# Kernel optimization log

Hardware: AMD Instinct MI355X
Metric: run time of the kernel (lower is better)

The kernel has to match this reference:

```python
import jax, jax.numpy as jnp
import numpy as np

N = 50000      # nodes
E = 1600000    # edges (before self loops)
IN = 128
OUT = 128
H = 4
HD = OUT // H  # head dim = 32


def setup_inputs() -> dict:
    key = jax.random.key(0)
    k1, k2, k3, k4, k5 = jax.random.split(key, 5)
    x = jax.random.normal(k1, (N, IN), dtype=jnp.float32)
    edge_index = jax.random.randint(k2, (2, E), 0, N, dtype=jnp.int64)
    # xavier-uniform-ish scales
    W = jax.random.normal(k3, (OUT, IN), dtype=jnp.float32) * (1.0 / np.sqrt(IN))
    att_src = jax.random.normal(k4, (1, H, HD), dtype=jnp.float32) * 0.1
    att_dst = jax.random.normal(k5, (1, H, HD), dtype=jnp.float32) * 0.1
    return {"x": x, "edge_index": edge_index, "W": W, "att_src": att_src, "att_dst": att_dst}


def reference(x, edge_index, W, att_src, att_dst):
    n = x.shape[0]
    # add self loops (tg.utils.add_self_loops appends [i, i] edges)
    loops = jnp.arange(n, dtype=edge_index.dtype)
    ei = jnp.concatenate([edge_index, jnp.stack([loops, loops])], axis=1)
    src, dst = ei[0], ei[1]

    # linear projection, split into heads: [n, H, HD]
    h = (x @ W.T).reshape(n, H, HD)

    # per-node attention logits per head: [n, H]
    a_src = jnp.sum(h * att_src, axis=-1)
    a_dst = jnp.sum(h * att_dst, axis=-1)

    # per-edge attention score: gather + leaky_relu
    alpha = a_src[src] + a_dst[dst]                      # [Etot, H]
    alpha = jax.nn.leaky_relu(alpha, negative_slope=0.2)

    # segment softmax grouped by destination node (numerically stable)
    m = jax.ops.segment_max(alpha, dst, num_segments=n)  # [n, H]
    e = jnp.exp(alpha - m[dst])
    s = jax.ops.segment_sum(e, dst, num_segments=n)      # [n, H]
    e = e / s[dst]                                       # [Etot, H]

    # weighted scatter-add aggregation; f_additive adds 1 to the weights
    msg = h[src] * (e[:, :, None] + 1.0)                 # [Etot, H, HD]
    out = jax.ops.segment_sum(msg, dst, num_segments=n)  # [n, H, HD]
    return out.reshape(n, -1)
```

## Files before the change

### kernel.cpp

```cpp
#include <hip/hip_runtime.h>

#define N_NODES 50000
#define E_EDGES 1600000
#define ETOT    (E_EDGES + N_NODES)
#define DIN  128
#define DOUT 128
#define NH   4
#define HD   32

typedef unsigned short ushort_t;
typedef unsigned int uint_t;
typedef __attribute__((ext_vector_type(8))) short bfrag;
typedef __attribute__((ext_vector_type(4))) float ffrag;

__device__ __forceinline__ ushort_t f2bf(float f) {
  uint_t u = __float_as_uint(f);
  u += 0x7fffu + ((u >> 16) & 1u);
  return (ushort_t)(u >> 16);
}
__device__ __forceinline__ float bf_lo(uint_t u) {
  return __uint_as_float(u << 16);
}
__device__ __forceinline__ float bf_hi(uint_t u) {
  return __uint_as_float(u & 0xffff0000u);
}

#define BSZ   64
#define NBUCK ((N_NODES + BSZ - 1) / BSZ)
#define NBP   1024
#define CAP   2560
#define EPB_A 8192
#define NBLK_A ((ETOT + EPB_A - 1) / EPB_A)
#define NCHUNK 13


__global__ __launch_bounds__(256, 4) void fused_binA_gemm_kernel(
    const int* __restrict__ ei, uint_t* __restrict__ ebuf,
    int* __restrict__ cntm, int* __restrict__ offm,
    const float* __restrict__ x, const float* __restrict__ W,
    const float* __restrict__ att_src, const float* __restrict__ att_dst,
    ushort_t* __restrict__ hb, float* __restrict__ a_src,
    float* __restrict__ a_dst) {
  __shared__ uint_t lds[EPB_A + NBP + 8];
  const int tid = threadIdx.x;

  if (blockIdx.x < NBLK_A) {
    uint_t* stage = lds;
    int* hist = (int*)(lds + EPB_A);
    int* wsum = hist + NBP;
    const int cb = blockIdx.x;
    const int e0 = cb * EPB_A;
    const int n = min(EPB_A, ETOT - e0);
    for (int i = tid; i < NBP; i += 256) hist[i] = 0;
    __syncthreads();
    for (int i = tid; i < n; i += 256) {
      int e = e0 + i;
      int si, di;
      if (e < E_EDGES) { si = ei[e]; di = ei[E_EDGES + e]; }
      else             { si = e - E_EDGES; di = si; }
      stage[i] = ((uint_t)di << 16) | (uint_t)si;
      atomicAdd(&hist[di >> 6], 1);
    }
    __syncthreads();
    const int ln = tid & 63, wv = tid >> 6;
    int c0 = hist[4 * tid], c1 = hist[4 * tid + 1];
    int c2 = hist[4 * tid + 2], c3 = hist[4 * tid + 3];
    int p1 = c0, p2 = c0 + c1, p3 = c0 + c1 + c2;
    int tot = p3 + c3;
    int xx = tot;
#pragma unroll
    for (int off = 1; off < 64; off <<= 1) {
      int y = __shfl_up(xx, off, 64);
      if (ln >= off) xx += y;
    }
    if (ln == 63) wsum[wv] = xx;
    __syncthreads();
    if (tid < 4) {
      int w = wsum[tid];
#pragma unroll
      for (int off = 1; off < 4; off <<= 1) {
        int y = __shfl_up(w, off, 64);
        if (tid >= off) w += y;
      }
      wsum[tid] = w;
    }
    __syncthreads();
    const int wo = (wv == 0) ? 0 : wsum[wv - 1];
    const int base = wo + xx - tot;
#pragma unroll
    for (int k = 0; k < 4; k++) {
      int idx = 4 * tid + k;
      int c = k == 0 ? c0 : k == 1 ? c1 : k == 2 ? c2 : c3;
      int o = base + (k == 0 ? 0 : k == 1 ? p1 : k == 2 ? p2 : p3);
      if (idx < NBUCK) {
        cntm[(size_t)cb * NBP + idx] = c;
        offm[(size_t)cb * NBP + idx] = o;
      }
      hist[idx] = o;
    }
    __syncthreads();
    for (int i = tid; i < n; i += 256) {
      uint_t p = stage[i];
      int pos = atomicAdd(&hist[p >> 22], 1);
      if (pos >= 0 && pos < n) ebuf[e0 + pos] = p;
    }
    return;
  }

  ushort_t* Ws = (ushort_t*)lds;
  const int gb = blockIdx.x - NBLK_A;
  const int wv = tid >> 6, l = tid & 63;
  const int lr = l & 15, lg = l >> 4;
  const int nbase = gb * 64 + wv * 16;
  int na = nbase + lr;
  if (na >= N_NODES) na = N_NODES - 1;
  const float* xrow = x + (size_t)na * DIN;

  float4 px[8];
#pragma unroll
  for (int kt = 0; kt < 4; kt++) {
    px[kt * 2]     = *(const float4*)&xrow[kt * 32 + lg * 8];
    px[kt * 2 + 1] = *(const float4*)&xrow[kt * 32 + lg * 8 + 4];
  }

  for (int u = tid; u < 2048; u += 256) {
    int row = u >> 4;
    float4 w0 = *(const float4*)&W[u * 8];
    float4 w1 = *(const float4*)&W[u * 8 + 4];
    uint4 pk;
    pk.x = (uint_t)f2bf(w0.x) | ((uint_t)f2bf(w0.y) << 16);
    pk.y = (uint_t)f2bf(w0.z) | ((uint_t)f2bf(w0.w) << 16);
    pk.z = (uint_t)f2bf(w1.x) | ((uint_t)f2bf(w1.y) << 16);
    pk.w = (uint_t)f2bf(w1.z) | ((uint_t)f2bf(w1.w) << 16);
    *(uint4*)&Ws[(u ^ (row & 7)) * 8] = pk;
  }
  __syncthreads();

  ffrag acc[8];
#pragma unroll
  for (int oc = 0; oc < 8; oc++) acc[oc] = (ffrag){0.f, 0.f, 0.f, 0.f};

#pragma unroll
  for (int kt = 0; kt < 4; kt++) {
    const float4 x0 = px[kt * 2];
    const float4 x1 = px[kt * 2 + 1];
    bfrag a;
    a[0] = (short)f2bf(x0.x); a[1] = (short)f2bf(x0.y);
    a[2] = (short)f2bf(x0.z); a[3] = (short)f2bf(x0.w);
    a[4] = (short)f2bf(x1.x); a[5] = (short)f2bf(x1.y);
    a[6] = (short)f2bf(x1.z); a[7] = (short)f2bf(x1.w);
#pragma unroll
    for (int oc = 0; oc < 8; oc++) {
      const int u = ((oc * 16 + lr) << 4) + kt * 4 + lg;
      const bfrag b = *(const bfrag*)&Ws[(u ^ (lr & 7)) * 8];
      acc[oc] = __builtin_amdgcn_mfma_f32_16x16x32_bf16(a, b, acc[oc], 0, 0, 0);
    }
  }

#pragma unroll
  for (int oc = 0; oc < 8; oc++) {
#pragma unroll
    for (int j = 0; j < 4; j++) {
      int n = nbase + lg * 4 + j;
      if (n < N_NODES)
        hb[((size_t)n << 7) + oc * 16 + lr] = f2bf(acc[oc][j]);
    }
  }

  float asv[8], adv[8];
#pragma unroll
  for (int oc = 0; oc < 8; oc++) {
    asv[oc] = att_src[oc * 16 + lr];
    adv[oc] = att_dst[oc * 16 + lr];
  }
#pragma unroll
  for (int j = 0; j < 4; j++) {
    float ps[4] = {0.f, 0.f, 0.f, 0.f};
    float pd[4] = {0.f, 0.f, 0.f, 0.f};
#pragma unroll
    for (int oc = 0; oc < 8; oc++) {
      ps[oc >> 1] = fmaf(acc[oc][j], asv[oc], ps[oc >> 1]);
      pd[oc >> 1] = fmaf(acc[oc][j], adv[oc], pd[oc >> 1]);
    }
#pragma unroll
    for (int off = 1; off < 16; off <<= 1) {
#pragma unroll
      for (int hd = 0; hd < 4; hd++) {
        ps[hd] += __shfl_xor(ps[hd], off);
        pd[hd] += __shfl_xor(pd[hd], off);
      }
    }
    int n = nbase + lg * 4 + j;
    if (n < N_NODES && lr < 4) {
      float vs = lr == 0 ? ps[0] : lr == 1 ? ps[1] : lr == 2 ? ps[2] : ps[3];
      float vd = lr == 0 ? pd[0] : lr == 1 ? pd[1] : lr == 2 ? pd[2] : pd[3];
      a_src[n * NH + lr] = vs;
      a_dst[n * NH + lr] = vd;
    }
  }
}

__global__ __launch_bounds__(256) void binB_kernel(
    const uint_t* __restrict__ ebuf, const int* __restrict__ cntm,
    const int* __restrict__ offm,
    int* __restrict__ rs, int* __restrict__ re, int* __restrict__ col) {
  __shared__ uint_t el[CAP];
  __shared__ int cnt_l[BSZ * NCHUNK];
  __shared__ int roff_l[BSZ * NCHUNK];
  __shared__ int wsum[4];
  const int b = blockIdx.x;
  const int tid = threadIdx.x;
  const int ln = tid & 63, wv = tid >> 6;
  const int n0 = b << 6;
  const int nn = min(BSZ, N_NODES - n0);

  int c = (tid < NBLK_A) ? cntm[(size_t)tid * NBP + b] : 0;
  int o = (tid < NBLK_A) ? offm[(size_t)tid * NBP + b] : 0;
  int xx = c;
#pragma unroll
  for (int off = 1; off < 64; off <<= 1) {
    int y = __shfl_up(xx, off, 64);
    if (ln >= off) xx += y;
  }
  if (ln == 63) wsum[wv] = xx;
  __syncthreads();
  if (tid < 4) {
    int w = wsum[tid];
#pragma unroll
    for (int off = 1; off < 4; off <<= 1) {
      int y = __shfl_up(w, off, 64);
      if (tid >= off) w += y;
    }
    wsum[tid] = w;
  }
  __syncthreads();
  const int wo = (wv == 0) ? 0 : wsum[wv - 1];
  const int mystart = wo + xx - c;
  const int total0 = wsum[3];
  const int total = total0 < CAP ? total0 : CAP;
  if (tid < NBLK_A) {
    const uint_t* src = ebuf + (size_t)tid * EPB_A + o;
    for (int j = 0; j < c; j++) {
      int d = mystart + j;
      if (d < CAP) el[d] = src[j];
    }
  }
  for (int k = tid; k < BSZ * NCHUNK; k += 256) cnt_l[k] = 0;
  __syncthreads();

  for (int i = tid; i < total; i += 256) {
    uint_t p = el[i];
    int key = (int)((p >> 16) & 63) * NCHUNK + (int)((p & 0xFFFFu) >> 12);
    atomicAdd(&cnt_l[key], 1);
  }
  __syncthreads();
  if (tid < BSZ) {
    int pref[NCHUNK];
    int tot = 0;
#pragma unroll
    for (int k = 0; k < NCHUNK; k++) { pref[k] = tot; tot += cnt_l[tid * NCHUNK + k]; }
    int x2 = tot;
#pragma unroll
    for (int off = 1; off < 64; off <<= 1) {
      int y = __shfl_up(x2, off, 64);
      if (tid >= off) x2 += y;
    }
    const int nodebase = x2 - tot;
#pragma unroll
    for (int k = 0; k < NCHUNK; k++) roff_l[tid * NCHUNK + k] = nodebase + pref[k];
    if (tid < nn) {
      rs[n0 + tid] = b * CAP + nodebase;
      re[n0 + tid] = b * CAP + nodebase + tot;
    }
  }
  __syncthreads();
  for (int k = tid; k < BSZ * NCHUNK; k += 256) cnt_l[k] = 0;
  __syncthreads();
  for (int i = tid; i < total; i += 256) {
    uint_t p = el[i];
    int si = (int)(p & 0xFFFFu);
    int key = (int)((p >> 16) & 63) * NCHUNK + (si >> 12);
    int pos = atomicAdd(&cnt_l[key], 1);
    int q = b * CAP + roff_l[key] + pos;
    if (q >= 0 && q < NBUCK * CAP) col[q] = si;
  }
}

#define NPB 16
#define CH  16

__global__ __launch_bounds__(256, 8) void agg_kernel(
    const int* __restrict__ col, const int* __restrict__ rs,
    const int* __restrict__ re, const ushort_t* __restrict__ hb,
    const float* __restrict__ a_src, const float* __restrict__ a_dst,
    float* __restrict__ out) {
  __shared__ float w_lds[NPB][CH][NH];
  __shared__ int   si_lds[NPB][CH];
  const int tid  = threadIdx.x;
  const int slot = tid >> 4;
  const int t    = tid & 15;
  const int node = blockIdx.x * NPB + slot;
  const int start = rs[node];
  const int deg   = re[node] - start;
  const float4 ad = *(const float4*)(a_dst + (size_t)node * NH);

  const int head = t >> 2;
  const int c8 = t << 3;
  const ushort_t* hc = hb + c8;
  float s = 0.f;
  float a0 = 0.f, a1 = 0.f, a2 = 0.f, a3 = 0.f;
  float a4 = 0.f, a5 = 0.f, a6 = 0.f, a7 = 0.f;
  float b0 = 0.f, b1 = 0.f, b2 = 0.f, b3 = 0.f;
  float b4 = 0.f, b5 = 0.f, b6 = 0.f, b7 = 0.f;

  for (int base_e = 0; base_e < deg; base_e += CH) {
    int nch = deg - base_e;
    if (nch > CH) nch = CH;
    if (t < nch) {
      int si = col[start + base_e + t];
      si = si < N_NODES ? si : 0;
      si_lds[slot][t] = si;
      float4 as = *(const float4*)(a_src + (size_t)si * NH);
      float v0 = as.x + ad.x; v0 = v0 > 0.f ? v0 : 0.2f * v0;
      float v1 = as.y + ad.y; v1 = v1 > 0.f ? v1 : 0.2f * v1;
      float v2 = as.z + ad.z; v2 = v2 > 0.f ? v2 : 0.2f * v2;
      float v3 = as.w + ad.w; v3 = v3 > 0.f ? v3 : 0.2f * v3;
      w_lds[slot][t][0] = __expf(v0);
      w_lds[slot][t][1] = __expf(v1);
      w_lds[slot][t][2] = __expf(v2);
      w_lds[slot][t][3] = __expf(v3);
    }
    __builtin_amdgcn_fence(__ATOMIC_ACQ_REL, "wavefront");
#pragma unroll 2
    for (int j = 0; j < nch; j++) {
      int si = si_lds[slot][j];
      float e = w_lds[slot][j][head];
      s += e;
      const uint4 hv = *(const uint4*)(hc + ((size_t)si << 7));
      float h0 = bf_lo(hv.x), h1 = bf_hi(hv.x);
      float h2 = bf_lo(hv.y), h3 = bf_hi(hv.y);
      float h4 = bf_lo(hv.z), h5 = bf_hi(hv.z);
      float h6 = bf_lo(hv.w), h7 = bf_hi(hv.w);
      a0 = fmaf(h0, e, a0); b0 += h0;
      a1 = fmaf(h1, e, a1); b1 += h1;
      a2 = fmaf(h2, e, a2); b2 += h2;
      a3 = fmaf(h3, e, a3); b3 += h3;
      a4 = fmaf(h4, e, a4); b4 += h4;
      a5 = fmaf(h5, e, a5); b5 += h5;
      a6 = fmaf(h6, e, a6); b6 += h6;
      a7 = fmaf(h7, e, a7); b7 += h7;
    }
    __builtin_amdgcn_fence(__ATOMIC_ACQ_REL, "wavefront");
  }
  const float inv = 1.0f / s;
  float* op = out + ((size_t)node << 7) + c8;
  *(float4*)(op)     = make_float4(fmaf(a0, inv, b0), fmaf(a1, inv, b1),
                                   fmaf(a2, inv, b2), fmaf(a3, inv, b3));
  *(float4*)(op + 4) = make_float4(fmaf(a4, inv, b4), fmaf(a5, inv, b5),
                                   fmaf(a6, inv, b6), fmaf(a7, inv, b7));
}

extern "C" void kernel_launch(void* const* d_in, const int* in_sizes, int n_in,
                              void* d_out, int out_size, void* d_ws, size_t ws_size,
                              hipStream_t stream) {
  const float* x       = (const float*)d_in[0];
  const int*   ei      = (const int*)d_in[1];
  const float* W       = (const float*)d_in[2];
  const float* att_src = (const float*)d_in[3];
  const float* att_dst = (const float*)d_in[4];
  float* out = (float*)d_out;

  ushort_t* hb = (ushort_t*)d_ws;
  float* a_src = (float*)(hb + (size_t)N_NODES * DOUT);
  float* a_dst = a_src + (size_t)N_NODES * NH;
  int* cntm    = (int*)(a_dst + (size_t)N_NODES * NH);
  int* offm    = cntm + (size_t)NBLK_A * NBP;
  int* rs      = offm + (size_t)NBLK_A * NBP;
  int* re      = rs + N_NODES;
  int* col     = re + N_NODES;
  uint_t* ebuf = (uint_t*)(col + (size_t)NBUCK * CAP);

  const int gemm_blocks = (N_NODES + 63) / 64;
  fused_binA_gemm_kernel<<<NBLK_A + gemm_blocks, 256, 0, stream>>>(
      ei, ebuf, cntm, offm, x, W, att_src, att_dst, hb, a_src, a_dst);
  binB_kernel<<<NBUCK, 256, 0, stream>>>(ebuf, cntm, offm, rs, re, col);
  agg_kernel<<<N_NODES / NPB, 256, 0, stream>>>(col, rs, re, hb, a_src, a_dst, out);
}
```

Before: 103.0 us.

## Split fused binning/GEMM kernel and prefetch next edge chunk in aggregation

Splits the fused edge-binning plus GEMM kernel into two separate launches. Each kernel now gets its own LDS footprint: the GEMM uses only a 32KB weight tile instead of the larger binning buffer, which could raise its occupancy. In the aggregation kernel, the next chunk's column index and a_src load are issued before the current chunk's gather loop, hiding that latency. This adds an extra kernel launch and gives up the overlap the fused launch provided between binning and GEMM.

```diff
diff --git a/kernel.cpp b/kernel.cpp
--- a/kernel.cpp
+++ b/kernel.cpp
@@ -34,81 +34,80 @@
 #define NCHUNK 13
 
 
-__global__ __launch_bounds__(256, 4) void fused_binA_gemm_kernel(
+__global__ __launch_bounds__(256) void binA2_kernel(
     const int* __restrict__ ei, uint_t* __restrict__ ebuf,
-    int* __restrict__ cntm, int* __restrict__ offm,
+    int* __restrict__ cntm, int* __restrict__ offm) {
+  __shared__ uint_t lds[EPB_A + NBP + 8];
+  uint_t* stage = lds;
+  int* hist = (int*)(lds + EPB_A);
+  int* wsum = hist + NBP;
+  const int tid = threadIdx.x;
+  const int cb = blockIdx.x;
+  const int e0 = cb * EPB_A;
+  const int n = min(EPB_A, ETOT - e0);
+  for (int i = tid; i < NBP; i += 256) hist[i] = 0;
+  __syncthreads();
+  for (int i = tid; i < n; i += 256) {
+    int e = e0 + i;
+    int si, di;
+    if (e < E_EDGES) { si = ei[e]; di = ei[E_EDGES + e]; }
+    else             { si = e - E_EDGES; di = si; }
+    stage[i] = ((uint_t)di << 16) | (uint_t)si;
+    atomicAdd(&hist[di >> 6], 1);
+  }
+  __syncthreads();
+  const int ln = tid & 63, wv = tid >> 6;
+  int c0 = hist[4 * tid], c1 = hist[4 * tid + 1];
+  int c2 = hist[4 * tid + 2], c3 = hist[4 * tid + 3];
+  int p1 = c0, p2 = c0 + c1, p3 = c0 + c1 + c2;
+  int tot = p3 + c3;
+  int xx = tot;
+#pragma unroll
+  for (int off = 1; off < 64; off <<= 1) {
+    int y = __shfl_up(xx, off, 64);
+    if (ln >= off) xx += y;
+  }
+  if (ln == 63) wsum[wv] = xx;
+  __syncthreads();
+  if (tid < 4) {
+    int w = wsum[tid];
+#pragma unroll
+    for (int off = 1; off < 4; off <<= 1) {
+      int y = __shfl_up(w, off, 64);
+      if (tid >= off) w += y;
+    }
+    wsum[tid] = w;
+  }
+  __syncthreads();
+  const int wo = (wv == 0) ? 0 : wsum[wv - 1];
+  const int base = wo + xx - tot;
+#pragma unroll
+  for (int k = 0; k < 4; k++) {
+    int idx = 4 * tid + k;
+    int c = k == 0 ? c0 : k == 1 ? c1 : k == 2 ? c2 : c3;
+    int o = base + (k == 0 ? 0 : k == 1 ? p1 : k == 2 ? p2 : p3);
+    if (idx < NBUCK) {
+      cntm[(size_t)cb * NBP + idx] = c;
+      offm[(size_t)cb * NBP + idx] = o;
+    }
+    hist[idx] = o;
+  }
+  __syncthreads();
+  for (int i = tid; i < n; i += 256) {
+    uint_t p = stage[i];
+    int pos = atomicAdd(&hist[p >> 22], 1);
+    if (pos >= 0 && pos < n) ebuf[e0 + pos] = p;
+  }
+}
+
+__global__ __launch_bounds__(256, 4) void gemm_att_kernel(
     const float* __restrict__ x, const float* __restrict__ W,
     const float* __restrict__ att_src, const float* __restrict__ att_dst,
     ushort_t* __restrict__ hb, float* __restrict__ a_src,
     float* __restrict__ a_dst) {
-  __shared__ uint_t lds[EPB_A + NBP + 8];
+  __shared__ ushort_t Ws[DIN * DOUT];
   const int tid = threadIdx.x;
-
-  if (blockIdx.x < NBLK_A) {
-    uint_t* stage = lds;
-    int* hist = (int*)(lds + EPB_A);
-    int* wsum = hist + NBP;
-    const int cb = blockIdx.x;
-    const int e0 = cb * EPB_A;
-    const int n = min(EPB_A, ETOT - e0);
-    for (int i = tid; i < NBP; i += 256) hist[i] = 0;
-    __syncthreads();
-    for (int i = tid; i < n; i += 256) {
-      int e = e0 + i;
-      int si, di;
-      if (e < E_EDGES) { si = ei[e]; di = ei[E_EDGES + e]; }
-      else             { si = e - E_EDGES; di = si; }
-      stage[i] = ((uint_t)di << 16) | (uint_t)si;
-      atomicAdd(&hist[di >> 6], 1);
-    }
-    __syncthreads();
-    const int ln = tid & 63, wv = tid >> 6;
-    int c0 = hist[4 * tid], c1 = hist[4 * tid + 1];
-    int c2 = hist[4 * tid + 2], c3 = hist[4 * tid + 3];
-    int p1 = c0, p2 = c0 + c1, p3 = c0 + c1 + c2;
-    int tot = p3 + c3;
-    int xx = tot;
-#pragma unroll
-    for (int off = 1; off < 64; off <<= 1) {
-      int y = __shfl_up(xx, off, 64);
-      if (ln >= off) xx += y;
-    }
-    if (ln == 63) wsum[wv] = xx;
-    __syncthreads();
-    if (tid < 4) {
-      int w = wsum[tid];
-#pragma unroll
-      for (int off = 1; off < 4; off <<= 1) {
-        int y = __shfl_up(w, off, 64);
-        if (tid >= off) w += y;
-      }
-      wsum[tid] = w;
-    }
-    __syncthreads();
-    const int wo = (wv == 0) ? 0 : wsum[wv - 1];
-    const int base = wo + xx - tot;
-#pragma unroll
-    for (int k = 0; k < 4; k++) {
-      int idx = 4 * tid + k;
-      int c = k == 0 ? c0 : k == 1 ? c1 : k == 2 ? c2 : c3;
-      int o = base + (k == 0 ? 0 : k == 1 ? p1 : k == 2 ? p2 : p3);
-      if (idx < NBUCK) {
-        cntm[(size_t)cb * NBP + idx] = c;
-        offm[(size_t)cb * NBP + idx] = o;
-      }
-      hist[idx] = o;
-    }
-    __syncthreads();
-    for (int i = tid; i < n; i += 256) {
-      uint_t p = stage[i];
-      int pos = atomicAdd(&hist[p >> 22], 1);
-      if (pos >= 0 && pos < n) ebuf[e0 + pos] = p;
-    }
-    return;
-  }
-
-  ushort_t* Ws = (ushort_t*)lds;
-  const int gb = blockIdx.x - NBLK_A;
+  const int gb = blockIdx.x;
   const int wv = tid >> 6, l = tid & 63;
   const int lr = l & 15, lg = l >> 4;
   const int nbase = gb * 64 + wv * 16;
@@ -313,24 +312,36 @@
   float b0 = 0.f, b1 = 0.f, b2 = 0.f, b3 = 0.f;
   float b4 = 0.f, b5 = 0.f, b6 = 0.f, b7 = 0.f;
 
+  int   si_c = 0;
+  float4 as_c = make_float4(0.f, 0.f, 0.f, 0.f);
+  if (t < deg) {
+    si_c = col[start + t];
+    si_c = si_c < N_NODES ? si_c : 0;
+    as_c = *(const float4*)(a_src + (size_t)si_c * NH);
+  }
+
   for (int base_e = 0; base_e < deg; base_e += CH) {
     int nch = deg - base_e;
     if (nch > CH) nch = CH;
     if (t < nch) {
-      int si = col[start + base_e + t];
-      si = si < N_NODES ? si : 0;
-      si_lds[slot][t] = si;
-      float4 as = *(const float4*)(a_src + (size_t)si * NH);
-      float v0 = as.x + ad.x; v0 = v0 > 0.f ? v0 : 0.2f * v0;
-      float v1 = as.y + ad.y; v1 = v1 > 0.f ? v1 : 0.2f * v1;
-      float v2 = as.z + ad.z; v2 = v2 > 0.f ? v2 : 0.2f * v2;
-      float v3 = as.w + ad.w; v3 = v3 > 0.f ? v3 : 0.2f * v3;
+      si_lds[slot][t] = si_c;
+      float v0 = as_c.x + ad.x; v0 = v0 > 0.f ? v0 : 0.2f * v0;
+      float v1 = as_c.y + ad.y; v1 = v1 > 0.f ? v1 : 0.2f * v1;
+      float v2 = as_c.z + ad.z; v2 = v2 > 0.f ? v2 : 0.2f * v2;
+      float v3 = as_c.w + ad.w; v3 = v3 > 0.f ? v3 : 0.2f * v3;
       w_lds[slot][t][0] = __expf(v0);
       w_lds[slot][t][1] = __expf(v1);
       w_lds[slot][t][2] = __expf(v2);
       w_lds[slot][t][3] = __expf(v3);
     }
     __builtin_amdgcn_fence(__ATOMIC_ACQ_REL, "wavefront");
+    int nb = base_e + CH;
+    if (nb + t < deg) {
+      int sn = col[start + nb + t];
+      sn = sn < N_NODES ? sn : 0;
+      si_c = sn;
+      as_c = *(const float4*)(a_src + (size_t)sn * NH);
+    }
 #pragma unroll 2
     for (int j = 0; j < nch; j++) {
       int si = si_lds[slot][j];
@@ -380,9 +391,9 @@
   int* col     = re + N_NODES;
   uint_t* ebuf = (uint_t*)(col + (size_t)NBUCK * CAP);
 
-  const int gemm_blocks = (N_NODES + 63) / 64;
-  fused_binA_gemm_kernel<<<NBLK_A + gemm_blocks, 256, 0, stream>>>(
-      ei, ebuf, cntm, offm, x, W, att_src, att_dst, hb, a_src, a_dst);
+  binA2_kernel<<<NBLK_A, 256, 0, stream>>>(ei, ebuf, cntm, offm);
+  gemm_att_kernel<<<(N_NODES + 63) / 64, 256, 0, stream>>>(
+      x, W, att_src, att_dst, hb, a_src, a_dst);
   binB_kernel<<<NBUCK, 256, 0, stream>>>(ebuf, cntm, offm, rs, re, col);
   agg_kernel<<<N_NODES / NPB, 256, 0, stream>>>(col, rs, re, hb, a_src, a_dst, out);
 }
```

After: 117.0 us. 13.6% more time.
